# Optimization experiments

Measured on AMD Instinct MI355X. Metric: run time of the kernel, lower is better.

The kernel has to match this reference:

```python
import jax, jax.numpy as jnp
import numpy as np

VOCABSIZE = 100000
EMBEDSIZE = 128
BATCH = 262144


def setup_inputs() -> dict:
    key = jax.random.key(0)
    k1, k2, k3, k4, k5 = jax.random.split(key, 5)
    xs = jax.random.randint(k1, (BATCH,), 0, VOCABSIZE, dtype=jnp.int64 if jax.config.jax_enable_x64 else jnp.int32)
    ys = jax.random.randint(k2, (BATCH,), 0, VOCABSIZE, dtype=jnp.int64 if jax.config.jax_enable_x64 else jnp.int32)
    metric = jax.random.normal(k3, (EMBEDSIZE, EMBEDSIZE), dtype=jnp.float32)
    EMBEDM = jax.random.normal(k4, (VOCABSIZE, EMBEDSIZE), dtype=jnp.float32)
    # Original inits NEGEMBEDM to zeros; we use small random values so the
    # output / gradients are non-degenerate for kernel correctness testing.
    NEGEMBEDM = jax.random.normal(k5, (VOCABSIZE, EMBEDSIZE), dtype=jnp.float32) * 0.1
    return {"xs": xs, "ys": ys, "metric": metric, "EMBEDM": EMBEDM, "NEGEMBEDM": NEGEMBEDM}


def reference(xs, ys, metric, EMBEDM, NEGEMBEDM):
    # Faithful math: diag((E[xs] @ metric) @ N[ys].T) == sum((E[xs] @ metric) * N[ys], -1).
    # We compute the batched bilinear form directly, avoiding the O(B^2*D)
    # full matmul + diag extraction of the original.
    xsembeds = EMBEDM[xs]          # [B, D]
    ysembeds = NEGEMBEDM[ys]       # [B, D]
    d = jnp.einsum('bd,de,be->b', xsembeds, metric, ysembeds)  # [B]
    return jax.nn.sigmoid(2.0 * d - 1.0)
```

## Files before the change

kernel.cpp:

```cpp
#include <hip/hip_runtime.h>
#include <hip/hip_fp16.h>

#define D        128
#define NROWS    100000
#define NET      (NROWS / 16)
#define NUNITS   (2 * NET)
#define GRID_P   768
#define NWAVES   (GRID_P * 4)

typedef __attribute__((ext_vector_type(8))) _Float16 f16x8;
typedef __attribute__((ext_vector_type(4))) _Float16 f16x4;
typedef __attribute__((ext_vector_type(4))) float    f32x4;

union F16x8U { _Float16 h[8]; f16x8 v; };
union F16x4U { _Float16 h[4]; f16x4 v; };
union F32x4U { float f[4]; f32x4 v; };

typedef __attribute__((address_space(1))) const void gvoid;
typedef __attribute__((address_space(3))) void       lvoid;

__global__ __launch_bounds__(256) void convert_M16(
    const float* __restrict__ M, _Float16* __restrict__ mh)
{
    const int q    = blockIdx.x * 256 + threadIdx.x;
    const int kk   = q >> 9;
    const int cf   = (q >> 6) & 7;
    const int lane = q & 63;
    const int col  = cf * 16 + (lane & 15);
    const int k0   = kk * 32 + (lane >> 4) * 8;

    F16x8U h;
    #pragma unroll
    for (int j = 0; j < 8; ++j) h.h[j] = (_Float16)M[(k0 + j) * D + col];
    *(f16x8*)(mh + q * 8) = h.v;
}

__global__ __launch_bounds__(256, 3) void prep_all2(
    const float* __restrict__ E, const float* __restrict__ N,
    const _Float16* __restrict__ mh,
    _Float16* __restrict__ Ep, _Float16* __restrict__ Np)
{
    __shared__ _Float16 smM[2048 * 8];
    __shared__ _Float16 scr[4][2048];

    const int tid  = threadIdx.x;
    const int lane = tid & 63;
    const int w    = tid >> 6;
    const int lrow = lane & 15;
    const int lk   = lane >> 4;

    #pragma unroll
    for (int it = 0; it < 8; ++it) {
        const int slot = it * 256 + w * 64 + lane;
        __builtin_amdgcn_global_load_lds(
            (gvoid*)(mh + slot * 8), (lvoid*)(smM + (it * 256 + w * 64) * 8),
            16, 0, 0);
    }
    asm volatile("s_waitcnt vmcnt(0)" ::: "memory");
    __syncthreads();

    const f16x8* Bh = (const f16x8*)smM;
    _Float16*    S  = scr[w];

    const int gw = (int)blockIdx.x * 4 + w;

    #pragma unroll 1
    for (int u = gw; u < NUNITS; u += NWAVES) {
        const int t16 = u >> 1;

        if ((u & 1) == 0) {
            #pragma unroll
            for (int i = 0; i < 8; ++i) {
                const int f   = i * 256 + lane * 4;
                const int row = f >> 7;
                const int col = f & 127;
                F32x4U v; v.v = *(const f32x4*)(E + (size_t)t16 * 2048 + f);
                F16x4U h4;
                h4.h[0] = (_Float16)v.f[0]; h4.h[1] = (_Float16)v.f[1];
                h4.h[2] = (_Float16)v.f[2]; h4.h[3] = (_Float16)v.f[3];
                const int tsl = (col >> 3) ^ row;
                *(f16x4*)(S + row * 128 + tsl * 8 + (col & 7)) = h4.v;
            }
            asm volatile("s_waitcnt lgkmcnt(0)" ::: "memory");
            __builtin_amdgcn_sched_barrier(0);

            f32x4 acc[8];
            #pragma unroll
            for (int cf = 0; cf < 8; ++cf) acc[cf] = (f32x4){0.f, 0.f, 0.f, 0.f};

            #pragma unroll
            for (int kk = 0; kk < 4; ++kk) {
                const f16x8 a16 =
                    *(const f16x8*)(S + lrow * 128 + ((kk * 4 + lk) ^ lrow) * 8);
                #pragma unroll
                for (int cf = 0; cf < 8; ++cf)
                    acc[cf] = __builtin_amdgcn_mfma_f32_16x16x32_f16(
                        a16, Bh[(kk * 8 + cf) * 64 + lane], acc[cf], 0, 0, 0);
            }

            #pragma unroll
            for (int i = 0; i < 4; ++i) {
                const int ro = t16 * 16 + lk * 4 + i;
                F16x8U o;
                #pragma unroll
                for (int cf = 0; cf < 8; ++cf) o.h[cf] = (_Float16)acc[cf][i];
                *(f16x8*)(Ep + (size_t)ro * D + lrow * 8) = o.v;
            }
        } else {
            #pragma unroll
            for (int i = 0; i < 8; ++i) {
                const int f   = i * 256 + lane * 4;
                const int row = f >> 7;
                const int col = f & 127;
                F32x4U v; v.v = *(const f32x4*)(N + (size_t)t16 * 2048 + f);
                const int lo = col & 15;
                const int hi = col >> 4;
                _Float16* base = S + row * 128 + hi;
                base[(lo    ) * 8] = (_Float16)v.f[0];
                base[(lo + 1) * 8] = (_Float16)v.f[1];
                base[(lo + 2) * 8] = (_Float16)v.f[2];
                base[(lo + 3) * 8] = (_Float16)v.f[3];
            }
            asm volatile("s_waitcnt lgkmcnt(0)" ::: "memory");
            __builtin_amdgcn_sched_barrier(0);

            #pragma unroll
            for (int i = 0; i < 4; ++i) {
                const f16x8 t = *(const f16x8*)(S + i * 512 + lane * 8);
                *(f16x8*)(Np + (size_t)t16 * 2048 + i * 512 + lane * 8) = t;
            }
        }

    }
}

__global__ __launch_bounds__(256) void gather_dot16(
    const int* __restrict__ xs, const int* __restrict__ ys,
    const _Float16* __restrict__ Ep, const _Float16* __restrict__ Np,
    float* __restrict__ out)
{
    const int tid = threadIdx.x;
    const int o0  = blockIdx.x * 32 + (tid >> 4) * 2;
    const int l   = tid & 15;

    const int x0 = xs[o0], x1 = xs[o0 + 1];
    const int y0 = ys[o0], y1 = ys[o0 + 1];

    const f16x8 a0 = *(const f16x8*)(Ep + (size_t)x0 * D + l * 8);
    const f16x8 b0 = *(const f16x8*)(Np + (size_t)y0 * D + l * 8);
    const f16x8 a1 = *(const f16x8*)(Ep + (size_t)x1 * D + l * 8);
    const f16x8 b1 = *(const f16x8*)(Np + (size_t)y1 * D + l * 8);

    float r0 = 0.f, r1 = 0.f;
    #pragma unroll
    for (int j = 0; j < 8; ++j) {
        r0 += (float)a0[j] * (float)b0[j];
        r1 += (float)a1[j] * (float)b1[j];
    }

    r0 += __shfl_xor(r0, 1); r1 += __shfl_xor(r1, 1);
    r0 += __shfl_xor(r0, 2); r1 += __shfl_xor(r1, 2);
    r0 += __shfl_xor(r0, 4); r1 += __shfl_xor(r1, 4);
    r0 += __shfl_xor(r0, 8); r1 += __shfl_xor(r1, 8);

    if (l == 0) {
        float2 v;
        v.x = 1.0f / (1.0f + __expf(1.0f - 2.0f * r0));
        v.y = 1.0f / (1.0f + __expf(1.0f - 2.0f * r1));
        *(float2*)(out + o0) = v;
    }
}

extern "C" void kernel_launch(void* const* d_in, const int* in_sizes, int n_in,
                              void* d_out, int out_size, void* d_ws, size_t ws_size,
                              hipStream_t stream) {
    const int*   xs     = (const int*)d_in[0];
    const int*   ys     = (const int*)d_in[1];
    const float* metric = (const float*)d_in[2];
    const float* EMBEDM = (const float*)d_in[3];
    const float* NEGEM  = (const float*)d_in[4];
    float*       out    = (float*)d_out;

    const int B = in_sizes[0];

    char* ws = (char*)d_ws;
    _Float16* Np = (_Float16*)ws;
    _Float16* Ep = (_Float16*)(ws + (32u << 20));
    _Float16* mh = (_Float16*)(ws + (64u << 20));

    convert_M16<<<8, 256, 0, stream>>>(metric, mh);

    prep_all2<<<GRID_P, 256, 0, stream>>>(EMBEDM, NEGEM, mh, Ep, Np);

    gather_dot16<<<B / 32, 256, 0, stream>>>(xs, ys, Ep, Np, out);
}
```

Baseline: 52.09 us.

## Drop NEGEMBEDM fp16 preconversion and gather fp32 rows directly in dot kernel

```diff
diff --git a/kernel.cpp b/kernel.cpp
--- a/kernel.cpp
+++ b/kernel.cpp
@@ -4,7 +4,6 @@
 #define D        128
 #define NROWS    100000
 #define NET      (NROWS / 16)
-#define NUNITS   (2 * NET)
 #define GRID_P   768
 #define NWAVES   (GRID_P * 4)
 
@@ -35,10 +34,9 @@
     *(f16x8*)(mh + q * 8) = h.v;
 }
 
-__global__ __launch_bounds__(256, 3) void prep_all2(
-    const float* __restrict__ E, const float* __restrict__ N,
-    const _Float16* __restrict__ mh,
-    _Float16* __restrict__ Ep, _Float16* __restrict__ Np)
+__global__ __launch_bounds__(256, 3) void gemm_E_pers(
+    const float* __restrict__ E, const _Float16* __restrict__ mh,
+    _Float16* __restrict__ Ep)
 {
     __shared__ _Float16 smM[2048 * 8];
     __shared__ _Float16 scr[4][2048];
@@ -65,78 +63,50 @@
     const int gw = (int)blockIdx.x * 4 + w;
 
     #pragma unroll 1
-    for (int u = gw; u < NUNITS; u += NWAVES) {
-        const int t16 = u >> 1;
+    for (int t = gw; t < NET; t += NWAVES) {
+        #pragma unroll
+        for (int i = 0; i < 8; ++i) {
+            const int f   = i * 256 + lane * 4;
+            const int row = f >> 7;
+            const int col = f & 127;
+            F32x4U v; v.v = *(const f32x4*)(E + (size_t)t * 2048 + f);
+            F16x4U h4;
+            h4.h[0] = (_Float16)v.f[0]; h4.h[1] = (_Float16)v.f[1];
+            h4.h[2] = (_Float16)v.f[2]; h4.h[3] = (_Float16)v.f[3];
+            const int tsl = (col >> 3) ^ row;
+            *(f16x4*)(S + row * 128 + tsl * 8 + (col & 7)) = h4.v;
+        }
+        asm volatile("s_waitcnt lgkmcnt(0)" ::: "memory");
+        __builtin_amdgcn_sched_barrier(0);
 
-        if ((u & 1) == 0) {
+        f32x4 acc[8];
+        #pragma unroll
+        for (int cf = 0; cf < 8; ++cf) acc[cf] = (f32x4){0.f, 0.f, 0.f, 0.f};
+
+        #pragma unroll
+        for (int kk = 0; kk < 4; ++kk) {
+            const f16x8 a16 =
+                *(const f16x8*)(S + lrow * 128 + ((kk * 4 + lk) ^ lrow) * 8);
             #pragma unroll
-            for (int i = 0; i < 8; ++i) {
-                const int f   = i * 256 + lane * 4;
-                const int row = f >> 7;
-                const int col = f & 127;
-                F32x4U v; v.v = *(const f32x4*)(E + (size_t)t16 * 2048 + f);
-                F16x4U h4;
-                h4.h[0] = (_Float16)v.f[0]; h4.h[1] = (_Float16)v.f[1];
-                h4.h[2] = (_Float16)v.f[2]; h4.h[3] = (_Float16)v.f[3];
-                const int tsl = (col >> 3) ^ row;
-                *(f16x4*)(S + row * 128 + tsl * 8 + (col & 7)) = h4.v;
-            }
-            asm volatile("s_waitcnt lgkmcnt(0)" ::: "memory");
-            __builtin_amdgcn_sched_barrier(0);
-
-            f32x4 acc[8];
-            #pragma unroll
-            for (int cf = 0; cf < 8; ++cf) acc[cf] = (f32x4){0.f, 0.f, 0.f, 0.f};
-
-            #pragma unroll
-            for (int kk = 0; kk < 4; ++kk) {
-                const f16x8 a16 =
-                    *(const f16x8*)(S + lrow * 128 + ((kk * 4 + lk) ^ lrow) * 8);
-                #pragma unroll
-                for (int cf = 0; cf < 8; ++cf)
-                    acc[cf] = __builtin_amdgcn_mfma_f32_16x16x32_f16(
-                        a16, Bh[(kk * 8 + cf) * 64 + lane], acc[cf], 0, 0, 0);
-            }
-
-            #pragma unroll
-            for (int i = 0; i < 4; ++i) {
-                const int ro = t16 * 16 + lk * 4 + i;
-                F16x8U o;
-                #pragma unroll
-                for (int cf = 0; cf < 8; ++cf) o.h[cf] = (_Float16)acc[cf][i];
-                *(f16x8*)(Ep + (size_t)ro * D + lrow * 8) = o.v;
-            }
-        } else {
-            #pragma unroll
-            for (int i = 0; i < 8; ++i) {
-                const int f   = i * 256 + lane * 4;
-                const int row = f >> 7;
-                const int col = f & 127;
-                F32x4U v; v.v = *(const f32x4*)(N + (size_t)t16 * 2048 + f);
-                const int lo = col & 15;
-                const int hi = col >> 4;
-                _Float16* base = S + row * 128 + hi;
-                base[(lo    ) * 8] = (_Float16)v.f[0];
-                base[(lo + 1) * 8] = (_Float16)v.f[1];
-                base[(lo + 2) * 8] = (_Float16)v.f[2];
-                base[(lo + 3) * 8] = (_Float16)v.f[3];
-            }
-            asm volatile("s_waitcnt lgkmcnt(0)" ::: "memory");
-            __builtin_amdgcn_sched_barrier(0);
-
-            #pragma unroll
-            for (int i = 0; i < 4; ++i) {
-                const f16x8 t = *(const f16x8*)(S + i * 512 + lane * 8);
-                *(f16x8*)(Np + (size_t)t16 * 2048 + i * 512 + lane * 8) = t;
-            }
+            for (int cf = 0; cf < 8; ++cf)
+                acc[cf] = __builtin_amdgcn_mfma_f32_16x16x32_f16(
+                    a16, Bh[(kk * 8 + cf) * 64 + lane], acc[cf], 0, 0, 0);
         }
 
+        #pragma unroll
+        for (int i = 0; i < 4; ++i) {
+            const int ro = t * 16 + lk * 4 + i;
+            F16x8U o;
+            #pragma unroll
+            for (int cf = 0; cf < 8; ++cf) o.h[cf] = (_Float16)acc[cf][i];
+            *(f16x8*)(Ep + (size_t)ro * D + lrow * 8) = o.v;
+        }
     }
 }
 
-__global__ __launch_bounds__(256) void gather_dot16(
+__global__ __launch_bounds__(256) void gather_dotN(
     const int* __restrict__ xs, const int* __restrict__ ys,
-    const _Float16* __restrict__ Ep, const _Float16* __restrict__ Np,
+    const _Float16* __restrict__ Ep, const float* __restrict__ N,
     float* __restrict__ out)
 {
     const int tid = threadIdx.x;
@@ -147,15 +117,15 @@
     const int y0 = ys[o0], y1 = ys[o0 + 1];
 
     const f16x8 a0 = *(const f16x8*)(Ep + (size_t)x0 * D + l * 8);
-    const f16x8 b0 = *(const f16x8*)(Np + (size_t)y0 * D + l * 8);
     const f16x8 a1 = *(const f16x8*)(Ep + (size_t)x1 * D + l * 8);
-    const f16x8 b1 = *(const f16x8*)(Np + (size_t)y1 * D + l * 8);
+    const float* n0 = N + (size_t)y0 * D + l;
+    const float* n1 = N + (size_t)y1 * D + l;
 
     float r0 = 0.f, r1 = 0.f;
     #pragma unroll
     for (int j = 0; j < 8; ++j) {
-        r0 += (float)a0[j] * (float)b0[j];
-        r1 += (float)a1[j] * (float)b1[j];
+        r0 += (float)a0[j] * n0[16 * j];
+        r1 += (float)a1[j] * n1[16 * j];
     }
 
     r0 += __shfl_xor(r0, 1); r1 += __shfl_xor(r1, 1);
@@ -184,13 +154,12 @@
     const int B = in_sizes[0];
 
     char* ws = (char*)d_ws;
-    _Float16* Np = (_Float16*)ws;
-    _Float16* Ep = (_Float16*)(ws + (32u << 20));
+    _Float16* Ep = (_Float16*)ws;
     _Float16* mh = (_Float16*)(ws + (64u << 20));
 
     convert_M16<<<8, 256, 0, stream>>>(metric, mh);
 
-    prep_all2<<<GRID_P, 256, 0, stream>>>(EMBEDM, NEGEM, mh, Ep, Np);
+    gemm_E_pers<<<GRID_P, 256, 0, stream>>>(EMBEDM, mh, Ep);
 
-    gather_dot16<<<B / 32, 256, 0, stream>>>(xs, ys, Ep, Np, out);
+    gather_dotN<<<B / 32, 256, 0, stream>>>(xs, ys, Ep, NEGEM, out);
 }
```

Result: no change. 51.28 us (-1.6%).
